# Kernel optimization log

Hardware: AMD Instinct MI355X
Metric: run time of the kernel (lower is better)

Reference implementation:

```python
import jax, jax.numpy as jnp
import numpy as np

NUM_LAYERS = 4
INPUT_DIM = 512
BATCH = 16384


def setup_inputs() -> dict:
    key = jax.random.key(0)
    kx, kw, kb = jax.random.split(key, 3)
    x = jax.random.normal(kx, (BATCH, INPUT_DIM), dtype=jnp.float32)
    # PyTorch nn.Linear init: U(-1/sqrt(fan_in), 1/sqrt(fan_in))
    bound = 1.0 / np.sqrt(INPUT_DIM)
    W = jax.random.uniform(kw, (NUM_LAYERS, INPUT_DIM, INPUT_DIM), jnp.float32, -bound, bound)
    b = jax.random.uniform(kb, (NUM_LAYERS, INPUT_DIM), jnp.float32, -bound, bound)
    return {"x": x, "W": W, "b": b}


def reference(x, W, b):
    # x: [B, D]; W: [L, D, D] (torch Linear weight, so y = x @ W_i.T + b_i)
    x_list = [x]
    for i in range(NUM_LAYERS):
        x_ = x_list[-1]
        # sequentially accumulate dot-product residuals against all prior activations
        for x_pre in x_list[:-1]:
            s = jnp.sum(x_ * x_pre, axis=-1, keepdims=True)  # [B, 1]
            x_ = x_ + s
        y = jnp.einsum("bd,ed->be", x_, W[i]) + b[i]  # Linear: x_ @ W_i.T + b_i
        x_list.append(y)
    out = jnp.concatenate(x_list[1:], axis=-1)  # [B, L*D]
    return out
```

## Files before the change

### kernel.cpp

```cpp
#include <hip/hip_runtime.h>
#include <stdint.h>


#define BROWS 16384
#define DIM 512
#define NL 4
#define OUTSTRIDE (NL * DIM)

#define BM 128
#define BN 128
#define BK 32
#define NT (DIM / BK)

typedef unsigned short ushort_t;
typedef __attribute__((ext_vector_type(8))) short bf16x8;
typedef __attribute__((ext_vector_type(4))) float f32x4;

__device__ inline ushort_t f32_to_bf16(float f) {
    union { float f; uint32_t u; } v; v.f = f;
    uint32_t u = v.u;
    uint32_t r = (u + 0x7fffu + ((u >> 16) & 1u)) >> 16;
    return (ushort_t)r;
}

__device__ inline float bf16_bits_to_f32(ushort_t u) {
    union { uint32_t u; float f; } v; v.u = ((uint32_t)u) << 16; return v.f;
}

__device__ inline float wave_reduce_sum(float v) {
    #pragma unroll
    for (int off = 32; off > 0; off >>= 1) v += __shfl_down(v, off, 64);
    return v;
}

__global__ __launch_bounds__(256) void prep_kernel(
    const float* __restrict__ W, const float* __restrict__ x0,
    ushort_t* __restrict__ Wb, float* __restrict__ wsum,
    ushort_t* __restrict__ xb0, float* __restrict__ sum0)
{
    int t = threadIdx.x;
    int wave = t >> 6, lane = t & 63;
    if (blockIdx.x < NL * DIM) {
        int row = blockIdx.x;
        const float* wp = W + (size_t)row * DIM;
        float f0 = wp[2 * t], f1 = wp[2 * t + 1];
        ushort_t* wbp = Wb + (size_t)row * DIM;
        wbp[2 * t]     = f32_to_bf16(f0);
        wbp[2 * t + 1] = f32_to_bf16(f1);
        __shared__ float red[4];
        float r = wave_reduce_sum(f0 + f1);
        if (lane == 0) red[wave] = r;
        __syncthreads();
        if (t == 0) wsum[row] = red[0] + red[1] + red[2] + red[3];
    } else {
        int b = (blockIdx.x - NL * DIM) * 4 + wave;
        const float* xp = x0 + (size_t)b * DIM + lane * 8;
        float4 a = ((const float4*)xp)[0];
        float4 c4 = ((const float4*)xp)[1];
        float f[8] = {a.x, a.y, a.z, a.w, c4.x, c4.y, c4.z, c4.w};
        bf16x8 o;
        float s = 0.f;
        #pragma unroll
        for (int i = 0; i < 8; ++i) {
            o[i] = (short)f32_to_bf16(f[i]);
            s += f[i];
        }
        *(bf16x8*)(xb0 + (size_t)b * DIM + lane * 8) = o;
        s = wave_reduce_sum(s);
        if (lane == 0) sum0[b] = s;
    }
}

template <int L, bool HASNEXT>
__global__ __launch_bounds__(256) void gemm_kernel(
    const ushort_t* __restrict__ xb,
    const ushort_t* __restrict__ Wb,
    const float* __restrict__ bias,
    const float* __restrict__ wsum,
    float* __restrict__ out,
    ushort_t* __restrict__ xb_next,
    const float* __restrict__ sum0,
    float* __restrict__ psum,
    float* __restrict__ pdot)
{
    __shared__ __align__(16) ushort_t sA[2][BM * BK];
    __shared__ __align__(16) ushort_t sB[2][BN * BK];
    __shared__ float sC[BM];

    int tid  = threadIdx.x;
    int wave = tid >> 6;
    int lane = tid & 63;
    int wm = wave >> 1, wn = wave & 1;

    int lid  = blockIdx.x;
    int xcd  = lid & 7, slot = lid >> 3;
    int orig = xcd * 64 + slot;
    int bx = orig & 3, by = orig >> 2;
    int bm = by * BM;
    int bn = bx * BN;

    const ushort_t* A = xb + (size_t)L * BROWS * DIM;

    f32x4 acc[4][4] = {};

    int srow = lane >> 2;
    int scol = (lane & 3) * 8;
    const ushort_t* gA0 = A  + (size_t)(bm + srow) * DIM + scol;
    const ushort_t* gB0 = Wb + (size_t)(bn + srow) * DIM + scol;

    auto stage = [&](int buf, int k0) {
        #pragma unroll
        for (int t2 = 0; t2 < 2; ++t2) {
            int r = wave * 32 + t2 * 16;
            __builtin_amdgcn_global_load_lds(
                (const __attribute__((address_space(1))) void*)(gA0 + (size_t)r * DIM + k0),
                (__attribute__((address_space(3))) void*)(&sA[buf][r * BK]), 16, 0, 0);
            __builtin_amdgcn_global_load_lds(
                (const __attribute__((address_space(1))) void*)(gB0 + (size_t)r * DIM + k0),
                (__attribute__((address_space(3))) void*)(&sB[buf][r * BK]), 16, 0, 0);
        }
    };

    stage(0, 0);
    __syncthreads();

    int q8 = (lane >> 4) * 8;
    int rr = lane & 15;
    for (int t = 0; t < NT; ++t) {
        int cur = t & 1;
        if (t + 1 < NT) stage(cur ^ 1, (t + 1) * BK);
        bf16x8 af[4], bfr[4];
        #pragma unroll
        for (int mi = 0; mi < 4; ++mi)
            af[mi] = *(const bf16x8*)(&sA[cur][(wm * 64 + mi * 16 + rr) * BK + q8]);
        #pragma unroll
        for (int ni = 0; ni < 4; ++ni)
            bfr[ni] = *(const bf16x8*)(&sB[cur][(wn * 64 + ni * 16 + rr) * BK + q8]);
        #pragma unroll
        for (int mi = 0; mi < 4; ++mi)
            #pragma unroll
            for (int ni = 0; ni < 4; ++ni)
                acc[mi][ni] = __builtin_amdgcn_mfma_f32_16x16x32_bf16(
                    af[mi], bfr[ni], acc[mi][ni], 0, 0, 0);
        __syncthreads();
    }

    if (L > 0) {
        if (tid < BM) {
            int row = bm + tid;
            float c = 0.f;
            #pragma unroll
            for (int j = 0; j < L; ++j) {
                constexpr int pb = L * (L - 1) / 2;
                const float* pd = pdot + ((size_t)(pb + j) * 8) * BROWS + row;
                float d = 0.f;
                #pragma unroll
                for (int p = 0; p < 8; ++p) d += pd[(size_t)p * BROWS];
                float sj;
                if (j == 0) sj = sum0[row];
                else {
                    const float* ps = psum + ((size_t)(j - 1) * 8) * BROWS + row;
                    sj = 0.f;
                    #pragma unroll
                    for (int p = 0; p < 8; ++p) sj += ps[(size_t)p * BROWS];
                }
                c = c + d + c * sj;
            }
            sC[tid] = c;
        }
        __syncthreads();
    }

    int q = lane >> 4, nlane = lane & 15;
    int pq = wn * 4 + bx;
    float ws4[4], bs4[4];
    #pragma unroll
    for (int ni = 0; ni < 4; ++ni) {
        int n_g = bn + wn * 64 + ni * 16 + nlane;
        ws4[ni] = wsum[n_g];
        bs4[ni] = bias[n_g];
    }
    #pragma unroll
    for (int mi = 0; mi < 4; ++mi) {
        #pragma unroll
        for (int r = 0; r < 4; ++r) {
            int mloc = wm * 64 + mi * 16 + q * 4 + r;
            int m_g = bm + mloc;
            float c = (L > 0) ? sC[mloc] : 0.f;
            float vsum = 0.f, vdot0 = 0.f, vdot1 = 0.f, vdot2 = 0.f;
            #pragma unroll
            for (int ni = 0; ni < 4; ++ni) {
                int n_g = bn + wn * 64 + ni * 16 + nlane;
                float v = acc[mi][ni][r] + c * ws4[ni] + bs4[ni];
                out[(size_t)m_g * OUTSTRIDE + n_g] = v;
                if constexpr (HASNEXT) {
                    xb_next[(size_t)m_g * DIM + n_g] = f32_to_bf16(v);
                    vsum += v;
                    vdot0 += v * bf16_bits_to_f32(xb[((size_t)0 * BROWS + m_g) * DIM + n_g]);
                    if (L >= 1)
                        vdot1 += v * bf16_bits_to_f32(xb[((size_t)1 * BROWS + m_g) * DIM + n_g]);
                    if (L >= 2)
                        vdot2 += v * bf16_bits_to_f32(xb[((size_t)2 * BROWS + m_g) * DIM + n_g]);
                }
            }
            if constexpr (HASNEXT) {
                #pragma unroll
                for (int off = 8; off > 0; off >>= 1) {
                    vsum  += __shfl_xor(vsum,  off, 64);
                    vdot0 += __shfl_xor(vdot0, off, 64);
                    if (L >= 1) vdot1 += __shfl_xor(vdot1, off, 64);
                    if (L >= 2) vdot2 += __shfl_xor(vdot2, off, 64);
                }
                if (nlane == 0) {
                    constexpr int pbn = (L + 1) * L / 2;
                    psum[((size_t)L * 8 + pq) * BROWS + m_g] = vsum;
                    pdot[((size_t)(pbn + 0) * 8 + pq) * BROWS + m_g] = vdot0;
                    if (L >= 1) pdot[((size_t)(pbn + 1) * 8 + pq) * BROWS + m_g] = vdot1;
                    if (L >= 2) pdot[((size_t)(pbn + 2) * 8 + pq) * BROWS + m_g] = vdot2;
                }
            }
        }
    }
}

extern "C" void kernel_launch(void* const* d_in, const int* in_sizes, int n_in,
                              void* d_out, int out_size, void* d_ws, size_t ws_size,
                              hipStream_t stream) {
    (void)in_sizes; (void)n_in; (void)out_size; (void)ws_size;
    const float* x0   = (const float*)d_in[0];
    const float* W    = (const float*)d_in[1];
    const float* bias = (const float*)d_in[2];
    float* out = (float*)d_out;

    char* ws = (char*)d_ws;
    ushort_t* xb   = (ushort_t*)ws;
    ushort_t* Wb   = (ushort_t*)(ws + 67108864);
    float*    wsum = (float*)   (ws + 69206016);
    float*    sum0 = (float*)   (ws + 69214208);
    float*    psum = (float*)   (ws + 69279744);
    float*    pdot = (float*)   (ws + 70852608);

    prep_kernel<<<NL * DIM + BROWS / 4, 256, 0, stream>>>(W, x0, Wb, wsum, xb, sum0);

    const int nblk = (BROWS / BM) * (DIM / BN);
    gemm_kernel<0, true><<<nblk, 256, 0, stream>>>(
        xb, Wb, bias, wsum, out,
        xb + (size_t)1 * BROWS * DIM, sum0, psum, pdot);
    gemm_kernel<1, true><<<nblk, 256, 0, stream>>>(
        xb, Wb + (size_t)1 * DIM * DIM, bias + DIM, wsum + DIM, out + DIM,
        xb + (size_t)2 * BROWS * DIM, sum0, psum, pdot);
    gemm_kernel<2, true><<<nblk, 256, 0, stream>>>(
        xb, Wb + (size_t)2 * DIM * DIM, bias + 2 * DIM, wsum + 2 * DIM, out + 2 * DIM,
        xb + (size_t)3 * BROWS * DIM, sum0, psum, pdot);
    gemm_kernel<3, false><<<nblk, 256, 0, stream>>>(
        xb, Wb + (size_t)3 * DIM * DIM, bias + 3 * DIM, wsum + 3 * DIM, out + 3 * DIM,
        nullptr, sum0, psum, pdot);
}
```

Baseline: 257.4 us.

## Halve GEMM M-tile and use triple-buffered LDS pipeline with single barrier

Reduces the block tile from 128x128 to 64x128, doubling the block count for better CU occupancy and load balance, and updates the XCD remapping and per-wave fragment counts to match. The k-loop becomes a three-stage LDS ring with prefetch distance two, using explicit vmcnt waits and one barrier per iteration in place of the two syncthreads. The smaller tile lowers register use but increases redundant B-matrix loads per output element, and the partial-sum index pq is reordered to match.

```diff
diff --git a/kernel.cpp b/kernel.cpp
--- a/kernel.cpp
+++ b/kernel.cpp
@@ -7,10 +7,11 @@
 #define NL 4
 #define OUTSTRIDE (NL * DIM)
 
-#define BM 128
+#define BM 64
 #define BN 128
 #define BK 32
 #define NT (DIM / BK)
+#define NBUF 3
 
 typedef unsigned short ushort_t;
 typedef __attribute__((ext_vector_type(8))) short bf16x8;
@@ -83,8 +84,8 @@
     float* __restrict__ psum,
     float* __restrict__ pdot)
 {
-    __shared__ __align__(16) ushort_t sA[2][BM * BK];
-    __shared__ __align__(16) ushort_t sB[2][BN * BK];
+    __shared__ __align__(16) ushort_t sA[NBUF][BM * BK];
+    __shared__ __align__(16) ushort_t sB[NBUF][BN * BK];
     __shared__ float sC[BM];
 
     int tid  = threadIdx.x;
@@ -94,14 +95,14 @@
 
     int lid  = blockIdx.x;
     int xcd  = lid & 7, slot = lid >> 3;
-    int orig = xcd * 64 + slot;
+    int orig = xcd * 128 + slot;
     int bx = orig & 3, by = orig >> 2;
     int bm = by * BM;
     int bn = bx * BN;
 
     const ushort_t* A = xb + (size_t)L * BROWS * DIM;
 
-    f32x4 acc[4][4] = {};
+    f32x4 acc[2][4] = {};
 
     int srow = lane >> 2;
     int scol = (lane & 3) * 8;
@@ -109,40 +110,48 @@
     const ushort_t* gB0 = Wb + (size_t)(bn + srow) * DIM + scol;
 
     auto stage = [&](int buf, int k0) {
+        int ra = wave * 16;
+        __builtin_amdgcn_global_load_lds(
+            (const __attribute__((address_space(1))) void*)(gA0 + (size_t)ra * DIM + k0),
+            (__attribute__((address_space(3))) void*)(&sA[buf][ra * BK]), 16, 0, 0);
         #pragma unroll
         for (int t2 = 0; t2 < 2; ++t2) {
-            int r = wave * 32 + t2 * 16;
+            int rb = wave * 32 + t2 * 16;
             __builtin_amdgcn_global_load_lds(
-                (const __attribute__((address_space(1))) void*)(gA0 + (size_t)r * DIM + k0),
-                (__attribute__((address_space(3))) void*)(&sA[buf][r * BK]), 16, 0, 0);
-            __builtin_amdgcn_global_load_lds(
-                (const __attribute__((address_space(1))) void*)(gB0 + (size_t)r * DIM + k0),
-                (__attribute__((address_space(3))) void*)(&sB[buf][r * BK]), 16, 0, 0);
+                (const __attribute__((address_space(1))) void*)(gB0 + (size_t)rb * DIM + k0),
+                (__attribute__((address_space(3))) void*)(&sB[buf][rb * BK]), 16, 0, 0);
         }
     };
 
     stage(0, 0);
-    __syncthreads();
+    stage(1, BK);
 
     int q8 = (lane >> 4) * 8;
     int rr = lane & 15;
     for (int t = 0; t < NT; ++t) {
-        int cur = t & 1;
-        if (t + 1 < NT) stage(cur ^ 1, (t + 1) * BK);
-        bf16x8 af[4], bfr[4];
-        #pragma unroll
-        for (int mi = 0; mi < 4; ++mi)
-            af[mi] = *(const bf16x8*)(&sA[cur][(wm * 64 + mi * 16 + rr) * BK + q8]);
+        int cur = t % 3;
+        if (t < NT - 1) {
+            asm volatile("s_waitcnt vmcnt(3)" ::: "memory");
+        } else {
+            asm volatile("s_waitcnt vmcnt(0)" ::: "memory");
+        }
+        __builtin_amdgcn_s_barrier();
+        __builtin_amdgcn_sched_barrier(0);
+        if (t + 2 < NT) stage((t + 2) % 3, (t + 2) * BK);
+
+        bf16x8 af[2], bfr[4];
+        #pragma unroll
+        for (int mi = 0; mi < 2; ++mi)
+            af[mi] = *(const bf16x8*)(&sA[cur][(wm * 32 + mi * 16 + rr) * BK + q8]);
         #pragma unroll
         for (int ni = 0; ni < 4; ++ni)
             bfr[ni] = *(const bf16x8*)(&sB[cur][(wn * 64 + ni * 16 + rr) * BK + q8]);
         #pragma unroll
-        for (int mi = 0; mi < 4; ++mi)
+        for (int mi = 0; mi < 2; ++mi)
             #pragma unroll
             for (int ni = 0; ni < 4; ++ni)
                 acc[mi][ni] = __builtin_amdgcn_mfma_f32_16x16x32_bf16(
                     af[mi], bfr[ni], acc[mi][ni], 0, 0, 0);
-        __syncthreads();
     }
 
     if (L > 0) {
@@ -172,7 +181,7 @@
     }
 
     int q = lane >> 4, nlane = lane & 15;
-    int pq = wn * 4 + bx;
+    int pq = bx * 2 + wn;
     float ws4[4], bs4[4];
     #pragma unroll
     for (int ni = 0; ni < 4; ++ni) {
@@ -181,10 +190,10 @@
         bs4[ni] = bias[n_g];
     }
     #pragma unroll
-    for (int mi = 0; mi < 4; ++mi) {
+    for (int mi = 0; mi < 2; ++mi) {
         #pragma unroll
         for (int r = 0; r < 4; ++r) {
-            int mloc = wm * 64 + mi * 16 + q * 4 + r;
+            int mloc = wm * 32 + mi * 16 + q * 4 + r;
             int m_g = bm + mloc;
             float c = (L > 0) ? sC[mloc] : 0.f;
             float vsum = 0.f, vdot0 = 0.f, vdot1 = 0.f, vdot2 = 0.f;
```

Result: faster. 251.5 us (-2.3%).
